# Optimization experiments

Hardware: AMD Instinct MI355X
Metric: run time of the kernel (lower is better)

Reference implementation:

```python
import jax, jax.numpy as jnp
import numpy as np

B, C, T = 8, 512, 1024
H = 8
D = C // H          # head_dim = 64
K = 64              # max_rel_dist
REL = 2 * K + 1     # 129


def setup_inputs() -> dict:
    key = jax.random.key(0)
    ks = jax.random.split(key, 12)
    s = 0.02
    return {
        "x": jax.random.normal(ks[0], (B, C, T), jnp.float32),
        "x_mask": jnp.ones((B, 1, T), jnp.float32),
        "W_q": jax.random.normal(ks[1], (C, C), jnp.float32) * s,
        "b_q": jnp.zeros((C,), jnp.float32),
        "W_k": jax.random.normal(ks[2], (C, C), jnp.float32) * s,
        "b_k": jnp.zeros((C,), jnp.float32),
        "W_v": jax.random.normal(ks[3], (C, C), jnp.float32) * s,
        "b_v": jnp.zeros((C,), jnp.float32),
        "W_o": jax.random.normal(ks[4], (C, C), jnp.float32) * s,
        "b_o": jnp.zeros((C,), jnp.float32),
        "emb_rel_k": jax.random.normal(ks[5], (REL, D), jnp.float32) * 0.01,
        "emb_rel_v": jax.random.normal(ks[6], (REL, D), jnp.float32) * 0.01,
    }


def _conv1x1(x, W, b):
    # Conv1d with kernel_size=1: (B,C,T) x (Cout,Cin) -> (B,Cout,T)
    return jnp.einsum("oc,bct->bot", W, x) + b[None, :, None]


def _shape_heads(x):
    # (B,C,T) -> (B,H,T,D)
    b = x.shape[0]
    return x.reshape(b, H, D, T).transpose(0, 1, 3, 2)


def reference(x, x_mask, W_q, b_q, W_k, b_k, W_v, b_v, W_o, b_o, emb_rel_k, emb_rel_v):
    q = _shape_heads(_conv1x1(x, W_q, b_q))  # (B,H,T,D)
    k = _shape_heads(_conv1x1(x, W_k, b_k))
    v = _shape_heads(_conv1x1(x, W_v, b_v))

    # relative position indices: clamp(j - i, -K, K) + K  -> (T,T)
    pos = jnp.arange(T)
    rel_idx = jnp.clip(pos[None, :] - pos[:, None], -K, K) + K

    # scores: scaled QK^T plus unscaled relative-key term (faithful to source)
    attn = jnp.einsum("bhid,bhjd->bhij", q, k) / (D ** 0.5)
    rel_k_tt = emb_rel_k[rel_idx]            # (T,T,D)
    attn = attn + jnp.einsum("bhid,ijd->bhij", q, rel_k_tt)

    # key mask: positions with x_mask <= 0 get -1e9
    key_mask = (x_mask <= 0).reshape(x.shape[0], 1, 1, T)
    attn = jnp.where(key_mask, -1e9, attn)
    attn = jax.nn.softmax(attn, axis=-1)     # dropout p=0.0 -> identity

    y = jnp.einsum("bhij,bhjd->bhid", attn, v)
    rel_v_tt = emb_rel_v[rel_idx]            # (T,T,D)
    y = y + jnp.einsum("bhij,ijd->bhid", attn, rel_v_tt)

    # (B,H,T,D) -> (B,H,D,T) -> (B,C,T)
    y = y.transpose(0, 1, 3, 2).reshape(x.shape[0], C, T)
    y = _conv1x1(y, W_o, b_o)
    return y * x_mask
```

## Files before the change

kernel.cpp:

```cpp
#include <hip/hip_runtime.h>

#define B_   8
#define C_   512
#define T_   1024
#define H_   8
#define D_   64
#define K_   64
#define REL_ 129

typedef unsigned short u16;
typedef __attribute__((ext_vector_type(8))) short short8;
typedef __attribute__((ext_vector_type(4))) float f32x4;

__device__ __forceinline__ float b2f(u16 u) {
    return __uint_as_float(((unsigned)u) << 16);
}
__device__ __forceinline__ u16 f2b(float f) {
    unsigned x = __float_as_uint(f);
    x += 0x7fffu + ((x >> 16) & 1u);
    return (u16)(x >> 16);
}

__global__ __launch_bounds__(256) void cast_all_kernel(
    const float* __restrict__ x,
    const float* __restrict__ Wq, const float* __restrict__ Wk,
    const float* __restrict__ Wv, const float* __restrict__ Wo,
    const float* __restrict__ erk, const float* __restrict__ erv,
    u16* __restrict__ xt, u16* __restrict__ Wh,
    u16* __restrict__ ervt, u16* __restrict__ erkb)
{
    __shared__ u16 tile[64][72];
    const int blk = blockIdx.x;
    const int tid = threadIdx.x;
    if (blk < 1024) {
        const int t0 = (blk & 15) * 64, c0 = ((blk >> 4) & 7) * 64, b = blk >> 7;
        const int f = tid & 15, r0 = tid >> 4;
#pragma unroll
        for (int p = 0; p < 4; ++p) {
            const int c = r0 + p * 16;
            const float4 v = *(const float4*)(x + ((size_t)b * C_ + c0 + c) * T_ + t0 + f * 4);
            tile[c][f * 4 + 0] = f2b(v.x);
            tile[c][f * 4 + 1] = f2b(v.y);
            tile[c][f * 4 + 2] = f2b(v.z);
            tile[c][f * 4 + 3] = f2b(v.w);
        }
        __syncthreads();
#pragma unroll
        for (int p = 0; p < 4; ++p) {
            const int t = r0 + p * 16;
            ushort4 u;
            u.x = tile[f * 4 + 0][t];
            u.y = tile[f * 4 + 1][t];
            u.z = tile[f * 4 + 2][t];
            u.w = tile[f * 4 + 3][t];
            *(ushort4*)(xt + ((size_t)b * T_ + t0 + t) * C_ + c0 + f * 4) = u;
        }
    } else if (blk < 2048) {
        const int gid = (blk - 1024) * 256 + tid;
        const int s = gid >> 16;
        const int off = (gid & 65535) * 4;
        const float* W = (s == 0) ? Wq : (s == 1) ? Wk : (s == 2) ? Wv : Wo;
        const float4 v = *(const float4*)(W + off);
        ushort4 u;
        u.x = f2b(v.x); u.y = f2b(v.y); u.z = f2b(v.z); u.w = f2b(v.w);
        *(ushort4*)(Wh + ((size_t)s << 18) + off) = u;
    } else {
        const int idx = (blk - 2048) * 256 + tid;
        if (idx < 64 * 160) {
            const int d = idx / 160, rel = idx % 160;
            ervt[idx] = (rel < REL_) ? f2b(erv[rel * D_ + d]) : (u16)0;
        } else {
            const int j = idx - 64 * 160;
            if (j < REL_ * D_) erkb[j] = f2b(erk[j]);
        }
    }
}

__global__ __launch_bounds__(256) void proj_mfma(
    const u16* __restrict__ xt, const u16* __restrict__ Wh,
    const float* __restrict__ bq, const float* __restrict__ bk, const float* __restrict__ bv,
    u16* __restrict__ qh, u16* __restrict__ kh, u16* __restrict__ vt)
{
    __shared__ u16 Wt[64][72];

    const int t0 = blockIdx.x * 64;
    const int h  = blockIdx.y;
    const int sel = blockIdx.z >> 3;
    const int b   = blockIdx.z & 7;
    const int tid = threadIdx.x, wave = tid >> 6, lane = tid & 63;
    const int quad = lane >> 4, l16 = lane & 15;

    const u16* Wbase = Wh + ((size_t)sel << 18) + ((size_t)(h * 64) << 9);
    const u16* A = xt + (((size_t)b * T_ + t0 + wave * 16 + l16) << 9);

    const int so = tid >> 2;
    const int sc = (tid & 3) * 16;
    const u16* wsrc = Wbase + ((size_t)so << 9) + sc;

    f32x4 acc[4] = {{0.f,0.f,0.f,0.f},{0.f,0.f,0.f,0.f},{0.f,0.f,0.f,0.f},{0.f,0.f,0.f,0.f}};

    uint4 wv0 = *(const uint4*)(wsrc);
    uint4 wv1 = *(const uint4*)(wsrc + 8);
#pragma unroll 1
    for (int i = 0; i < 8; ++i) {
        const int c0 = i * 64;
        __syncthreads();
        *(uint4*)&Wt[so][sc] = wv0;
        *(uint4*)&Wt[so][sc + 8] = wv1;
        __syncthreads();
        if (i < 7) {
            wv0 = *(const uint4*)(wsrc + c0 + 64);
            wv1 = *(const uint4*)(wsrc + c0 + 72);
        }
#pragma unroll
        for (int kk = 0; kk < 64; kk += 32) {
            const short8 af = *(const short8*)(A + c0 + kk + quad * 8);
#pragma unroll
            for (int nt = 0; nt < 4; ++nt) {
                const short8 bf = *(const short8*)(&Wt[nt * 16 + l16][kk + quad * 8]);
                acc[nt] = __builtin_amdgcn_mfma_f32_16x16x32_bf16(af, bf, acc[nt], 0, 0, 0);
            }
        }
    }

    const float* bias = (sel == 0) ? bq : (sel == 1) ? bk : bv;
    const int bh = b * 8 + h;
#pragma unroll
    for (int nt = 0; nt < 4; ++nt) {
        const int d = nt * 16 + l16;
        const float bo = bias[h * 64 + d];
#pragma unroll
        for (int rix = 0; rix < 4; ++rix) {
            const int t = t0 + wave * 16 + quad * 4 + rix;
            const u16 val = f2b(acc[nt][rix] + bo);
            if (sel == 2) {
                vt[(((size_t)bh * 64 + d) << 10) + t] = val;
            } else {
                u16* dst = sel ? kh : qh;
                dst[(((size_t)bh * T_ + t) << 6) + d] = val;
            }
        }
    }
}

__global__ __launch_bounds__(256, 2) void attn_kernel(
    const u16* __restrict__ qh, const u16* __restrict__ kh, const u16* __restrict__ vt,
    const u16* __restrict__ erkb, const u16* __restrict__ ervt,
    const float* __restrict__ xmask, u16* __restrict__ yf)
{
    __shared__ u16   Sb[32][1032];
    __shared__ u16   sw[32][168];
    __shared__ float red[4][32][2];
    __shared__ float invrow[32];

    const int gid = blockIdx.x;
    const int x8 = gid & 7, r5 = gid >> 3;
    const int bh = x8 + 8 * (r5 >> 5);
    const int i0 = (r5 & 31) * 32;
    const int b = bh >> 3, h = bh & 7;
    const int tid = threadIdx.x, wave = tid >> 6, lane = tid & 63;
    const int quad = lane >> 4, l16 = lane & 15;

    short8 qa[2][2];
#pragma unroll
    for (int g = 0; g < 2; ++g) {
        const u16* qrow = qh + (((size_t)bh * T_ + i0 + g * 16 + l16) << 6);
        qa[g][0] = *(const short8*)(qrow + quad * 8);
        qa[g][1] = *(const short8*)(qrow + 32 + quad * 8);
    }

    for (int tile = wave; tile < 9; tile += 4) {
        const int rel = tile * 16 + l16;
        const int rl = rel > 128 ? 128 : rel;
        const u16* ep = erkb + rl * 64 + quad * 8;
        const short8 b0 = *(const short8*)(ep);
        const short8 b1 = *(const short8*)(ep + 32);
#pragma unroll
        for (int g = 0; g < 2; ++g) {
            f32x4 m = {0.f, 0.f, 0.f, 0.f};
            m = __builtin_amdgcn_mfma_f32_16x16x32_bf16(qa[g][0], b0, m, 0, 0, 0);
            m = __builtin_amdgcn_mfma_f32_16x16x32_bf16(qa[g][1], b1, m, 0, 0, 0);
            if (rel < 129) {
#pragma unroll
                for (int rix = 0; rix < 4; ++rix)
                    sw[g * 16 + quad * 4 + rix][rel] = f2b(m[rix]);
            }
        }
    }
    __syncthreads();

    float slo_c[2][4], shi_c[2][4];
#pragma unroll
    for (int g = 0; g < 2; ++g)
#pragma unroll
        for (int rix = 0; rix < 4; ++rix) {
            const int row = g * 16 + quad * 4 + rix;
            slo_c[g][rix] = b2f(sw[row][0]);
            shi_c[g][rix] = b2f(sw[row][2 * K_]);
        }

    float psum[2][4] = {{0.f,0.f,0.f,0.f},{0.f,0.f,0.f,0.f}};
    float phi [2][4] = {{0.f,0.f,0.f,0.f},{0.f,0.f,0.f,0.f}};
    f32x4 og[4][2];
#pragma unroll
    for (int s = 0; s < 4; ++s)
#pragma unroll
        for (int g = 0; g < 2; ++g) og[s][g] = (f32x4){0.f, 0.f, 0.f, 0.f};

    {
        const u16* kb = kh + ((size_t)bh << 16);
        const u16* vbase = vt + ((size_t)bh << 16);
#pragma unroll 1
        for (int c = 0; c < 8; ++c) {
#pragma unroll
            for (int half = 0; half < 2; ++half) {
                const int ct = c * 2 + half;
                const int j0 = wave * 256 + ct * 16;
                const u16* krow = kb + ((size_t)(j0 + l16) << 6);
                const short8 kb0 = *(const short8*)(krow + quad * 8);
                const short8 kb1 = *(const short8*)(krow + 32 + quad * 8);
                const int j = j0 + l16;
                const float xmv = xmask[b * T_ + j];
#pragma unroll
                for (int g = 0; g < 2; ++g) {
                    f32x4 acc = {0.f, 0.f, 0.f, 0.f};
                    acc = __builtin_amdgcn_mfma_f32_16x16x32_bf16(qa[g][0], kb0, acc, 0, 0, 0);
                    acc = __builtin_amdgcn_mfma_f32_16x16x32_bf16(qa[g][1], kb1, acc, 0, 0, 0);
                    const int dd = j0 - (i0 + g * 16);
                    if (dd <= -79) {
#pragma unroll
                        for (int rix = 0; rix < 4; ++rix) {
                            const int row = g * 16 + quad * 4 + rix;
                            float val = acc[rix] * 0.125f + slo_c[g][rix];
                            val = (xmv > 0.f) ? val : -1e9f;
                            const u16 pb = f2b(__expf(fminf(val, 30.f)));
                            const float er = b2f(pb);
                            Sb[row][j] = pb;
                            psum[g][rix] += er;
                        }
                    } else if (dd >= 79) {
#pragma unroll
                        for (int rix = 0; rix < 4; ++rix) {
                            const int row = g * 16 + quad * 4 + rix;
                            float val = acc[rix] * 0.125f + shi_c[g][rix];
                            val = (xmv > 0.f) ? val : -1e9f;
                            const u16 pb = f2b(__expf(fminf(val, 30.f)));
                            const float er = b2f(pb);
                            Sb[row][j] = pb;
                            psum[g][rix] += er;
                            phi[g][rix]  += er;
                        }
                    } else {
#pragma unroll
                        for (int rix = 0; rix < 4; ++rix) {
                            const int row = g * 16 + quad * 4 + rix;
                            const int i = i0 + row;
                            int rel = j - i;
                            rel = (rel < -K_) ? -K_ : (rel > K_) ? K_ : rel;
                            float val = acc[rix] * 0.125f + b2f(sw[row][rel + K_]);
                            val = (xmv > 0.f) ? val : -1e9f;
                            const u16 pb = f2b(__expf(fminf(val, 30.f)));
                            const float er = b2f(pb);
                            Sb[row][j] = pb;
                            psum[g][rix] += er;
                            phi[g][rix]  += (j >= i + K_) ? er : 0.f;
                        }
                    }
                }
            }
            const int kc = wave * 256 + c * 32;
            const short8 pb0 = *(const short8*)(&Sb[l16][kc + quad * 8]);
            const short8 pb1 = *(const short8*)(&Sb[16 + l16][kc + quad * 8]);
#pragma unroll
            for (int s = 0; s < 4; ++s) {
                const short8 af = *(const short8*)(vbase + ((size_t)(s * 16 + l16) << 10) + kc + quad * 8);
                og[s][0] = __builtin_amdgcn_mfma_f32_16x16x32_bf16(af, pb0, og[s][0], 0, 0, 0);
                og[s][1] = __builtin_amdgcn_mfma_f32_16x16x32_bf16(af, pb1, og[s][1], 0, 0, 0);
            }
        }
#pragma unroll
        for (int m = 1; m < 16; m <<= 1)
#pragma unroll
            for (int g = 0; g < 2; ++g)
#pragma unroll
                for (int rix = 0; rix < 4; ++rix) {
                    psum[g][rix] += __shfl_xor(psum[g][rix], m);
                    phi[g][rix]  += __shfl_xor(phi[g][rix], m);
                }
        if (l16 == 0)
#pragma unroll
            for (int g = 0; g < 2; ++g)
#pragma unroll
                for (int rix = 0; rix < 4; ++rix) {
                    const int row = g * 16 + quad * 4 + rix;
                    red[wave][row][0] = psum[g][rix];
                    red[wave][row][1] = phi[g][rix];
                }
    }
    __syncthreads();

    {
        const int rr = tid >> 3;
        const int c0 = tid & 7;
        const float sumrow = red[0][rr][0] + red[1][rr][0] + red[2][rr][0] + red[3][rr][0];
        const float phirow = red[0][rr][1] + red[1][rr][1] + red[2][rr][1] + red[3][rr][1];
        float intsum = 0.f;
        for (int rel = c0; rel < 168; rel += 8) {
            if (rel == 0 || rel == 2 * K_) continue;
            u16 v = 0;
            if (rel < 2 * K_) {
                const int j = i0 + rr + rel - K_;
                if (j >= 0 && j < T_) v = Sb[rr][j];
                intsum += b2f(v);
            }
            sw[rr][rel] = v;
        }
        intsum += __shfl_xor(intsum, 1);
        intsum += __shfl_xor(intsum, 2);
        intsum += __shfl_xor(intsum, 4);
        if (c0 == 0) {
            sw[rr][2 * K_] = f2b(phirow);
            sw[rr][0]      = f2b(sumrow - intsum - phirow);
            invrow[rr]     = 1.0f / sumrow;
        }
    }
    __syncthreads();

    float* fog = (float*)&Sb[0][0];
#pragma unroll
    for (int s = 0; s < 4; ++s)
#pragma unroll
        for (int g = 0; g < 2; ++g)
            *(f32x4*)&fog[wave * 2048 + ((s * 2 + g) * 64 + lane) * 4] = og[s][g];
    __syncthreads();

    {
        const int dh = wave * 16 + l16;
        const u16* ep = ervt + dh * 160;
        f32x4 accg[2];
#pragma unroll
        for (int g = 0; g < 2; ++g) {
            const int base = ((wave * 2 + g) * 64 + lane) * 4;
            f32x4 a0 = *(const f32x4*)&fog[base];
            f32x4 a1 = *(const f32x4*)&fog[2048 + base];
            f32x4 a2 = *(const f32x4*)&fog[4096 + base];
            f32x4 a3 = *(const f32x4*)&fog[6144 + base];
#pragma unroll
            for (int rix = 0; rix < 4; ++rix)
                accg[g][rix] = (a0[rix] + a1[rix]) + (a2[rix] + a3[rix]);
        }
#pragma unroll
        for (int kt = 0; kt < 5; ++kt) {
            const short8 af = *(const short8*)(ep + kt * 32 + quad * 8);
            const short8 p0 = *(const short8*)(&sw[l16][kt * 32 + quad * 8]);
            const short8 p1 = *(const short8*)(&sw[16 + l16][kt * 32 + quad * 8]);
            accg[0] = __builtin_amdgcn_mfma_f32_16x16x32_bf16(af, p0, accg[0], 0, 0, 0);
            accg[1] = __builtin_amdgcn_mfma_f32_16x16x32_bf16(af, p1, accg[1], 0, 0, 0);
        }
        const int dbase = (h << 6) + wave * 16 + quad * 4;
#pragma unroll
        for (int g = 0; g < 2; ++g) {
            const float iv = invrow[g * 16 + l16];
            ushort4 u;
            u.x = f2b(accg[g][0] * iv); u.y = f2b(accg[g][1] * iv);
            u.z = f2b(accg[g][2] * iv); u.w = f2b(accg[g][3] * iv);
            *(ushort4*)(yf + (((size_t)b * T_ + i0 + g * 16 + l16) << 9) + dbase) = u;
        }
    }
}

__global__ __launch_bounds__(256) void outproj_mfma(
    const u16* __restrict__ yf, const u16* __restrict__ Woh, const float* __restrict__ bo,
    const float* __restrict__ xmask, float* __restrict__ out)
{
    __shared__ u16 Yt[64][72];

    const int o0 = blockIdx.x * 64;
    const int b  = blockIdx.y >> 4;
    const int t0 = (blockIdx.y & 15) * 64;
    const int tid = threadIdx.x, wave = tid >> 6, lane = tid & 63;
    const int quad = lane >> 4, l16 = lane & 15;

    const u16* A = Woh + ((size_t)(o0 + wave * 16 + l16) << 9);

    const int so = tid >> 2;
    const int sc = (tid & 3) * 16;
    const u16* ysrc = yf + (((size_t)b * T_ + t0 + so) << 9) + sc;

    f32x4 acc[4] = {{0.f,0.f,0.f,0.f},{0.f,0.f,0.f,0.f},{0.f,0.f,0.f,0.f},{0.f,0.f,0.f,0.f}};

    uint4 wv0 = *(const uint4*)(ysrc);
    uint4 wv1 = *(const uint4*)(ysrc + 8);
#pragma unroll 1
    for (int i = 0; i < 8; ++i) {
        const int c0 = i * 64;
        __syncthreads();
        *(uint4*)&Yt[so][sc] = wv0;
        *(uint4*)&Yt[so][sc + 8] = wv1;
        __syncthreads();
        if (i < 7) {
            wv0 = *(const uint4*)(ysrc + c0 + 64);
            wv1 = *(const uint4*)(ysrc + c0 + 72);
        }
#pragma unroll
        for (int kk = 0; kk < 64; kk += 32) {
            const short8 af = *(const short8*)(A + c0 + kk + quad * 8);
#pragma unroll
            for (int nt = 0; nt < 4; ++nt) {
                const short8 bf = *(const short8*)(&Yt[nt * 16 + l16][kk + quad * 8]);
                acc[nt] = __builtin_amdgcn_mfma_f32_16x16x32_bf16(af, bf, acc[nt], 0, 0, 0);
            }
        }
    }

#pragma unroll
    for (int nt = 0; nt < 4; ++nt) {
        const int t = t0 + nt * 16 + l16;
        const float xmv = xmask[b * T_ + t];
#pragma unroll
        for (int rix = 0; rix < 4; ++rix) {
            const int o = o0 + wave * 16 + quad * 4 + rix;
            out[((size_t)b * C_ + o) * T_ + t] = (acc[nt][rix] + bo[o]) * xmv;
        }
    }
}

extern "C" void kernel_launch(void* const* d_in, const int* in_sizes, int n_in,
                              void* d_out, int out_size, void* d_ws, size_t ws_size,
                              hipStream_t stream) {
    const float* x     = (const float*)d_in[0];
    const float* xmask = (const float*)d_in[1];
    const float* Wq    = (const float*)d_in[2];
    const float* bq    = (const float*)d_in[3];
    const float* Wk    = (const float*)d_in[4];
    const float* bk    = (const float*)d_in[5];
    const float* Wv    = (const float*)d_in[6];
    const float* bv    = (const float*)d_in[7];
    const float* Wo    = (const float*)d_in[8];
    const float* bo    = (const float*)d_in[9];
    const float* erk   = (const float*)d_in[10];
    const float* erv   = (const float*)d_in[11];

    const size_t need = 44077184;
    if (ws_size < need) return;
    u16* xt   = (u16*)d_ws;
    u16* Wh   = (u16*)((char*)d_ws + 8388608);
    u16* qh   = (u16*)((char*)d_ws + 10485760);
    u16* kh   = (u16*)((char*)d_ws + 18874368);
    u16* vt   = (u16*)((char*)d_ws + 27262976);
    u16* yf   = (u16*)((char*)d_ws + 35651584);
    u16* ervt = (u16*)((char*)d_ws + 44040192);
    u16* erkb = (u16*)((char*)d_ws + 44060672);
    float* out = (float*)d_out;

    cast_all_kernel<<<dim3(2121), 256, 0, stream>>>(
        x, Wq, Wk, Wv, Wo, erk, erv, xt, Wh, ervt, erkb);
    proj_mfma<<<dim3(T_ / 64, H_, 3 * B_), 256, 0, stream>>>(
        xt, Wh, bq, bk, bv, qh, kh, vt);
    attn_kernel<<<dim3(2048), 256, 0, stream>>>(
        qh, kh, vt, erkb, ervt, xmask, yf);
    outproj_mfma<<<dim3(C_ / 64, B_ * (T_ / 64)), 256, 0, stream>>>(
        yf, Wh + ((size_t)3 << 18), bo, xmask, out);
}
```

Before: 233.8 us.

## Split attention key range across eight waves and use exp2 with packed bf16 convert

Doubles the attention block to 512 threads so each wave processes half as many keys, widening the cross-wave reductions and the relative-value epilogue to match. The softmax exponent is rewritten as exp2 with log2e folded into the scale and the relative-key scores, and the mask is applied as a clamp bound. bf16 conversion of probabilities now uses a packed hardware convert. The aim is more latency hiding and fewer VALU ops per score, at the cost of more reduction work and higher register pressure under the new launch bounds.

Measured after the change: 244.4 us. +4.5%, slower.

```diff
diff --git a/kernel.cpp b/kernel.cpp
--- a/kernel.cpp
+++ b/kernel.cpp
@@ -143,14 +143,14 @@
     }
 }
 
-__global__ __launch_bounds__(256, 2) void attn_kernel(
+__global__ __launch_bounds__(512, 4) void attn_kernel(
     const u16* __restrict__ qh, const u16* __restrict__ kh, const u16* __restrict__ vt,
     const u16* __restrict__ erkb, const u16* __restrict__ ervt,
     const float* __restrict__ xmask, u16* __restrict__ yf)
 {
     __shared__ u16   Sb[32][1032];
     __shared__ u16   sw[32][168];
-    __shared__ float red[4][32][2];
+    __shared__ float red[8][32][2];
     __shared__ float invrow[32];
 
     const int gid = blockIdx.x;
@@ -161,6 +161,9 @@
     const int tid = threadIdx.x, wave = tid >> 6, lane = tid & 63;
     const int quad = lane >> 4, l16 = lane & 15;
 
+    const float LOG2E = 1.4426950408889634f;
+    const float SC    = 0.125f * 1.4426950408889634f;
+
     short8 qa[2][2];
 #pragma unroll
     for (int g = 0; g < 2; ++g) {
@@ -169,7 +172,7 @@
         qa[g][1] = *(const short8*)(qrow + 32 + quad * 8);
     }
 
-    for (int tile = wave; tile < 9; tile += 4) {
+    for (int tile = wave; tile < 9; tile += 8) {
         const int rel = tile * 16 + l16;
         const int rl = rel > 128 ? 128 : rel;
         const u16* ep = erkb + rl * 64 + quad * 8;
@@ -183,7 +186,7 @@
             if (rel < 129) {
 #pragma unroll
                 for (int rix = 0; rix < 4; ++rix)
-                    sw[g * 16 + quad * 4 + rix][rel] = f2b(m[rix]);
+                    sw[g * 16 + quad * 4 + rix][rel] = f2b(m[rix] * LOG2E);
             }
         }
     }
@@ -211,64 +214,73 @@
         const u16* kb = kh + ((size_t)bh << 16);
         const u16* vbase = vt + ((size_t)bh << 16);
 #pragma unroll 1
-        for (int c = 0; c < 8; ++c) {
+        for (int c = 0; c < 4; ++c) {
 #pragma unroll
             for (int half = 0; half < 2; ++half) {
                 const int ct = c * 2 + half;
-                const int j0 = wave * 256 + ct * 16;
+                const int j0 = wave * 128 + ct * 16;
                 const u16* krow = kb + ((size_t)(j0 + l16) << 6);
                 const short8 kb0 = *(const short8*)(krow + quad * 8);
                 const short8 kb1 = *(const short8*)(krow + 32 + quad * 8);
                 const int j = j0 + l16;
                 const float xmv = xmask[b * T_ + j];
+                const float clampv = (xmv > 0.f) ? 43.280850f : -2.0e9f;
 #pragma unroll
                 for (int g = 0; g < 2; ++g) {
                     f32x4 acc = {0.f, 0.f, 0.f, 0.f};
                     acc = __builtin_amdgcn_mfma_f32_16x16x32_bf16(qa[g][0], kb0, acc, 0, 0, 0);
                     acc = __builtin_amdgcn_mfma_f32_16x16x32_bf16(qa[g][1], kb1, acc, 0, 0, 0);
                     const int dd = j0 - (i0 + g * 16);
+                    const int ibase = i0 + g * 16 + quad * 4;
+                    float ee[4];
                     if (dd <= -79) {
 #pragma unroll
+                        for (int rix = 0; rix < 4; ++rix)
+                            ee[rix] = __builtin_amdgcn_exp2f(
+                                fminf(fmaf(acc[rix], SC, slo_c[g][rix]), clampv));
+                    } else if (dd >= 79) {
+#pragma unroll
+                        for (int rix = 0; rix < 4; ++rix)
+                            ee[rix] = __builtin_amdgcn_exp2f(
+                                fminf(fmaf(acc[rix], SC, shi_c[g][rix]), clampv));
+                    } else {
+                        const int relb = j - ibase + K_;
+#pragma unroll
                         for (int rix = 0; rix < 4; ++rix) {
+                            int idx = relb - rix;
+                            idx = idx < 0 ? 0 : (idx > 2 * K_ ? 2 * K_ : idx);
                             const int row = g * 16 + quad * 4 + rix;
-                            float val = acc[rix] * 0.125f + slo_c[g][rix];
-                            val = (xmv > 0.f) ? val : -1e9f;
-                            const u16 pb = f2b(__expf(fminf(val, 30.f)));
-                            const float er = b2f(pb);
-                            Sb[row][j] = pb;
-                            psum[g][rix] += er;
-                        }
-                    } else if (dd >= 79) {
-#pragma unroll
-                        for (int rix = 0; rix < 4; ++rix) {
-                            const int row = g * 16 + quad * 4 + rix;
-                            float val = acc[rix] * 0.125f + shi_c[g][rix];
-                            val = (xmv > 0.f) ? val : -1e9f;
-                            const u16 pb = f2b(__expf(fminf(val, 30.f)));
-                            const float er = b2f(pb);
-                            Sb[row][j] = pb;
-                            psum[g][rix] += er;
-                            phi[g][rix]  += er;
-                        }
-                    } else {
-#pragma unroll
-                        for (int rix = 0; rix < 4; ++rix) {
-                            const int row = g * 16 + quad * 4 + rix;
-                            const int i = i0 + row;
-                            int rel = j - i;
-                            rel = (rel < -K_) ? -K_ : (rel > K_) ? K_ : rel;
-                            float val = acc[rix] * 0.125f + b2f(sw[row][rel + K_]);
-                            val = (xmv > 0.f) ? val : -1e9f;
-                            const u16 pb = f2b(__expf(fminf(val, 30.f)));
-                            const float er = b2f(pb);
-                            Sb[row][j] = pb;
-                            psum[g][rix] += er;
-                            phi[g][rix]  += (j >= i + K_) ? er : 0.f;
+                            const float sr = b2f(sw[row][idx]);
+                            ee[rix] = __builtin_amdgcn_exp2f(
+                                fminf(fmaf(acc[rix], SC, sr), clampv));
                         }
                     }
+                    unsigned p01, p23;
+                    asm("v_cvt_pk_bf16_f32 %0, %1, %2" : "=v"(p01) : "v"(ee[0]), "v"(ee[1]));
+                    asm("v_cvt_pk_bf16_f32 %0, %1, %2" : "=v"(p23) : "v"(ee[2]), "v"(ee[3]));
+                    const int r0 = g * 16 + quad * 4;
+                    Sb[r0 + 0][j] = (u16)(p01 & 0xffffu);
+                    Sb[r0 + 1][j] = (u16)(p01 >> 16);
+                    Sb[r0 + 2][j] = (u16)(p23 & 0xffffu);
+                    Sb[r0 + 3][j] = (u16)(p23 >> 16);
+                    const float er0 = __uint_as_float(p01 << 16);
+                    const float er1 = __uint_as_float(p01 & 0xffff0000u);
+                    const float er2 = __uint_as_float(p23 << 16);
+                    const float er3 = __uint_as_float(p23 & 0xffff0000u);
+                    psum[g][0] += er0; psum[g][1] += er1;
+                    psum[g][2] += er2; psum[g][3] += er3;
+                    if (dd >= 79) {
+                        phi[g][0] += er0; phi[g][1] += er1;
+                        phi[g][2] += er2; phi[g][3] += er3;
+                    } else if (dd > -79) {
+                        phi[g][0] += (j - ibase >= 64) ? er0 : 0.f;
+                        phi[g][1] += (j - ibase >= 65) ? er1 : 0.f;
+                        phi[g][2] += (j - ibase >= 66) ? er2 : 0.f;
+                        phi[g][3] += (j - ibase >= 67) ? er3 : 0.f;
+                    }
                 }
             }
-            const int kc = wave * 256 + c * 32;
+            const int kc = wave * 128 + c * 32;
             const short8 pb0 = *(const short8*)(&Sb[l16][kc + quad * 8]);
             const short8 pb1 = *(const short8*)(&Sb[16 + l16][kc + quad * 8]);
 #pragma unroll
@@ -300,12 +312,16 @@
     __syncthreads();
 
     {
-        const int rr = tid >> 3;
-        const int c0 = tid & 7;
-        const float sumrow = red[0][rr][0] + red[1][rr][0] + red[2][rr][0] + red[3][rr][0];
-        const float phirow = red[0][rr][1] + red[1][rr][1] + red[2][rr][1] + red[3][rr][1];
+        const int rr = tid >> 4;
+        const int c0 = tid & 15;
+        float sumrow = 0.f, phirow = 0.f;
+#pragma unroll
+        for (int w = 0; w < 8; ++w) {
+            sumrow += red[w][rr][0];
+            phirow += red[w][rr][1];
+        }
         float intsum = 0.f;
-        for (int rel = c0; rel < 168; rel += 8) {
+        for (int rel = c0; rel < 168; rel += 16) {
             if (rel == 0 || rel == 2 * K_) continue;
             u16 v = 0;
             if (rel < 2 * K_) {
@@ -318,6 +334,7 @@
         intsum += __shfl_xor(intsum, 1);
         intsum += __shfl_xor(intsum, 2);
         intsum += __shfl_xor(intsum, 4);
+        intsum += __shfl_xor(intsum, 8);
         if (c0 == 0) {
             sw[rr][2 * K_] = f2b(phirow);
             sw[rr][0]      = f2b(sumrow - intsum - phirow);
@@ -335,37 +352,35 @@
     __syncthreads();
 
     {
-        const int dh = wave * 16 + l16;
+        const int s = wave >> 1, g = wave & 1;
+        const int dh = s * 16 + l16;
         const u16* ep = ervt + dh * 160;
-        f32x4 accg[2];
-#pragma unroll
-        for (int g = 0; g < 2; ++g) {
-            const int base = ((wave * 2 + g) * 64 + lane) * 4;
-            f32x4 a0 = *(const f32x4*)&fog[base];
-            f32x4 a1 = *(const f32x4*)&fog[2048 + base];
-            f32x4 a2 = *(const f32x4*)&fog[4096 + base];
-            f32x4 a3 = *(const f32x4*)&fog[6144 + base];
-#pragma unroll
-            for (int rix = 0; rix < 4; ++rix)
-                accg[g][rix] = (a0[rix] + a1[rix]) + (a2[rix] + a3[rix]);
-        }
+        const int base = ((s * 2 + g) * 64 + lane) * 4;
+        const f32x4 a0 = *(const f32x4*)&fog[0 * 2048 + base];
+        const f32x4 a1 = *(const f32x4*)&fog[1 * 2048 + base];
+        const f32x4 a2 = *(const f32x4*)&fog[2 * 2048 + base];
+        const f32x4 a3 = *(const f32x4*)&fog[3 * 2048 + base];
+        const f32x4 a4 = *(const f32x4*)&fog[4 * 2048 + base];
+        const f32x4 a5 = *(const f32x4*)&fog[5 * 2048 + base];
+        const f32x4 a6 = *(const f32x4*)&fog[6 * 2048 + base];
+        const f32x4 a7 = *(const f32x4*)&fog[7 * 2048 + base];
+        f32x4 accg;
+#pragma unroll
+        for (int rix = 0; rix < 4; ++rix)
+            accg[rix] = ((a0[rix] + a1[rix]) + (a2[rix] + a3[rix]))
+                      + ((a4[rix] + a5[rix]) + (a6[rix] + a7[rix]));
 #pragma unroll
         for (int kt = 0; kt < 5; ++kt) {
             const short8 af = *(const short8*)(ep + kt * 32 + quad * 8);
-            const short8 p0 = *(const short8*)(&sw[l16][kt * 32 + quad * 8]);
-            const short8 p1 = *(const short8*)(&sw[16 + l16][kt * 32 + quad * 8]);
-            accg[0] = __builtin_amdgcn_mfma_f32_16x16x32_bf16(af, p0, accg[0], 0, 0, 0);
-            accg[1] = __builtin_amdgcn_mfma_f32_16x16x32_bf16(af, p1, accg[1], 0, 0, 0);
-        }
-        const int dbase = (h << 6) + wave * 16 + quad * 4;
-#pragma unroll
-        for (int g = 0; g < 2; ++g) {
-            const float iv = invrow[g * 16 + l16];
-            ushort4 u;
-            u.x = f2b(accg[g][0] * iv); u.y = f2b(accg[g][1] * iv);
-            u.z = f2b(accg[g][2] * iv); u.w = f2b(accg[g][3] * iv);
-            *(ushort4*)(yf + (((size_t)b * T_ + i0 + g * 16 + l16) << 9) + dbase) = u;
-        }
+            const short8 p  = *(const short8*)(&sw[g * 16 + l16][kt * 32 + quad * 8]);
+            accg = __builtin_amdgcn_mfma_f32_16x16x32_bf16(af, p, accg, 0, 0, 0);
+        }
+        const int dbase = (h << 6) + s * 16 + quad * 4;
+        const float iv = invrow[g * 16 + l16];
+        ushort4 u;
+        u.x = f2b(accg[0] * iv); u.y = f2b(accg[1] * iv);
+        u.z = f2b(accg[2] * iv); u.w = f2b(accg[3] * iv);
+        *(ushort4*)(yf + (((size_t)b * T_ + i0 + g * 16 + l16) << 9) + dbase) = u;
     }
 }
 
@@ -457,7 +472,7 @@
         x, Wq, Wk, Wv, Wo, erk, erv, xt, Wh, ervt, erkb);
     proj_mfma<<<dim3(T_ / 64, H_, 3 * B_), 256, 0, stream>>>(
         xt, Wh, bq, bk, bv, qh, kh, vt);
-    attn_kernel<<<dim3(2048), 256, 0, stream>>>(
+    attn_kernel<<<dim3(2048), 512, 0, stream>>>(
         qh, kh, vt, erkb, ervt, xmask, yf);
     outproj_mfma<<<dim3(C_ / 64, B_ * (T_ / 64)), 256, 0, stream>>>(
         yf, Wh + ((size_t)3 << 18), bo, xmask, out);
```
